# Performance work log

Hardware: AMD Instinct MI355X
Metric: run time of the kernel (lower is better)

The kernel has to match this reference:

```python
import jax, jax.numpy as jnp
import numpy as np

BETA = 0.25

def setup_inputs() -> dict:
    key = jax.random.key(0)
    k1, k2 = jax.random.split(key)
    B, D, H, W = 32, 256, 32, 32
    K = 2048
    latents = jax.random.normal(k1, (B, D, H, W), dtype=jnp.float32)
    # torch init: uniform(-1/K, 1/K)
    embedding_weight = jax.random.uniform(k2, (K, D), dtype=jnp.float32, minval=-1.0 / K, maxval=1.0 / K)
    return {"latents": latents, "embedding_weight": embedding_weight}

def reference(latents, embedding_weight):
    B, D, H, W = latents.shape
    # NCHW -> NHWC -> (N, D)
    x = jnp.transpose(latents, (0, 2, 3, 1)).reshape(-1, D)
    dist = (jnp.sum(x * x, axis=1, keepdims=True)
            - 2.0 * jnp.matmul(x, embedding_weight.T)
            + jnp.sum(embedding_weight * embedding_weight, axis=1))
    embed_ind = jnp.argmin(dist, axis=1)  # argmax of -dist
    quantized = jnp.take(embedding_weight, embed_ind, axis=0)  # (N, D) gather, same math as onehot @ W
    x_nhwc = x.reshape(B, H, W, D)
    q_nhwc = quantized.reshape(B, H, W, D)
    # straight-through-style residual: latents + beta * (sg(quantized) - latents)
    out = x_nhwc + BETA * (jax.lax.stop_gradient(q_nhwc) - x_nhwc)
    out = jnp.transpose(out, (0, 3, 1, 2))  # back to NCHW
    return out, embed_ind.reshape(B, H, W)
```

## Files before the change

kernel.cpp:

```cpp
#include <hip/hip_runtime.h>
#include <math.h>

#define BB 32
#define DD 256
#define KK 2048
#define HW 1024
#define CHW (DD*HW)
#define NN (BB*HW)
#define BETA 0.25f
#define RROWS 32
#define NCAND 8
#define BIAS 0.125f

typedef __attribute__((ext_vector_type(8))) short short8v;
typedef __attribute__((ext_vector_type(4))) float f32x4;

typedef const __attribute__((address_space(1))) void gv_t;
typedef __attribute__((address_space(3))) void lv_t;

__device__ __forceinline__ void gl_lds16(const void* g, void* l) {
    __builtin_amdgcn_global_load_lds((gv_t*)g, (lv_t*)l, 16, 0, 0);
}

__device__ __forceinline__ unsigned bfr(float f) {
    unsigned u = __float_as_uint(f);
    return (u + 0x7FFFu + ((u >> 16) & 1u)) >> 16;
}
__device__ __forceinline__ unsigned bfpack(float lo, float hi) {
    return bfr(lo) | (bfr(hi) << 16);
}

#define BARRIER() do { asm volatile("" ::: "memory"); \
                       __builtin_amdgcn_s_barrier();  \
                       asm volatile("" ::: "memory"); } while (0)

__global__ __launch_bounds__(256) void k_prep(const float* __restrict__ E,
                                              uint4* __restrict__ EbfT,
                                              float* __restrict__ Cref,
                                              float* __restrict__ Ckey) {
    int bid = blockIdx.x;
    if (bid < 256) {
        int u = bid * 256 + threadIdx.x;
        int code = u & 31, kc = (u >> 5) & 3, c = (u >> 7) & 7, t = u >> 10;
        int k = t * 32 + code;
        const float* s = E + ((size_t)k * DD + c * 32 + kc * 8);
        float4 f0 = *reinterpret_cast<const float4*>(s);
        float4 f1 = *reinterpret_cast<const float4*>(s + 4);
        uint4 o;
        o.x = bfpack(f0.x, f0.y); o.y = bfpack(f0.z, f0.w);
        o.z = bfpack(f1.x, f1.y); o.w = bfpack(f1.z, f1.w);
        EbfT[u] = o;
    } else {
        const int w = threadIdx.x >> 6;
        const int lane = threadIdx.x & 63;
        const int k = (bid - 256) * 4 + w;
        float racc = 0.0f;
        if (lane < 16) {
#pragma clang fp contract(off)
            const int j = lane & 7, h = lane >> 3;
            const float* e = E + (size_t)k * DD + h * 128 + j;
            for (int i = 0; i < 16; ++i) {
                float t = e[i * 8];
                racc += t * t;
            }
        }
        float v0 = __shfl(racc, 0, 64),  v1 = __shfl(racc, 1, 64);
        float v2 = __shfl(racc, 2, 64),  v3 = __shfl(racc, 3, 64);
        float v4 = __shfl(racc, 4, 64),  v5 = __shfl(racc, 5, 64);
        float v6 = __shfl(racc, 6, 64),  v7 = __shfl(racc, 7, 64);
        float v8 = __shfl(racc, 8, 64),  v9 = __shfl(racc, 9, 64);
        float va = __shfl(racc, 10, 64), vb = __shfl(racc, 11, 64);
        float vc = __shfl(racc, 12, 64), vd = __shfl(racc, 13, 64);
        float ve = __shfl(racc, 14, 64), vf = __shfl(racc, 15, 64);
        if (lane == 0) {
#pragma clang fp contract(off)
            float lo = ((v0 + v1) + (v2 + v3)) + ((v4 + v5) + (v6 + v7));
            float hi = ((v8 + v9) + (va + vb)) + ((vc + vd) + (ve + vf));
            float res = lo + hi;
            Cref[k] = res;
            Ckey[k] = res + BIAS;
        }
    }
}

__global__ __launch_bounds__(512, 4) void k_screen(
        const float* __restrict__ X, const uint4* __restrict__ EbfT,
        const float* __restrict__ Ckey, uint2* __restrict__ ck)
{
    __shared__ __align__(1024) char lds[36864];

    const int tid = threadIdx.x;
    const int w = tid >> 6;
    const int rg = w >> 1;
    const int cg = w & 1;
    const int lane = tid & 63;
    const int lid = lane & 15, kc = lane >> 4;
    const int bid = blockIdx.x;
    const int half = bid & 1;
    const int tbase = half * 32;
    const int nb = (bid >> 1) * 64;
    const int b = nb >> 10;
    const int hw0 = nb & 1023;

    float* ckl = (float*)(lds + 32768);

    float ckg0 = Ckey[half * 1024 + tid];
    float ckg1 = Ckey[half * 1024 + 512 + tid];

    short8v a[8];
    {
        const float* xb = X + (size_t)b * CHW + (hw0 + rg * 16 + lid);
        #pragma unroll
        for (int c = 0; c < 8; ++c) {
            const float* pp = xb + (size_t)(c * 32 + kc * 8) * HW;
            float f[8];
            #pragma unroll
            for (int j = 0; j < 8; ++j) f[j] = pp[(size_t)j * HW];
            uint4 v;
            v.x = bfpack(f[0], f[1]); v.y = bfpack(f[2], f[3]);
            v.z = bfpack(f[4], f[5]); v.w = bfpack(f[6], f[7]);
            a[c] = *reinterpret_cast<short8v*>(&v);
        }
    }
    ckl[tid] = ckg0;
    ckl[tid + 512] = ckg1;

    auto stage = [&](int t, int p) {
        const uint4* src = EbfT + ((size_t)(tbase + t) * 1024 + w * 128 + lane);
        char* dst = lds + p * 16384 + (w * 128) * 16;
        #pragma unroll
        for (int i = 0; i < 2; ++i)
            gl_lds16(src + i * 64, dst + i * 1024);
    };
    stage(0, 0);
    stage(1, 1);
    asm volatile("s_waitcnt vmcnt(0) lgkmcnt(0)" ::: "memory");
    BARRIER();

    unsigned t1[4], t2[4];
    #pragma unroll
    for (int g = 0; g < 4; ++g) { t1[g] = 0xFFFFFFFFu; t2[g] = 0xFFFFFFFFu; }

    f32x4 acc = (f32x4){0.f, 0.f, 0.f, 0.f};

    int p = 0;
    float pck = 0.f;
    #pragma unroll 1
    for (int tt = 0; tt < 32; ++tt) {
        float ckv = ckl[tt * 32 + cg * 16 + lid];

        if (tt > 0) {
            unsigned tg = (unsigned)(tt - 1);
            #pragma unroll
            for (int g = 0; g < 4; ++g) {
                float s = fmaf(-2.0f, acc[g], pck);
                unsigned key = (__float_as_uint(s) & 0xFFFFFFE0u) | tg;
                unsigned o1 = t1[g];
                unsigned hi = key > o1 ? key : o1;
                t1[g] = key < o1 ? key : o1;
                t2[g] = hi < t2[g] ? hi : t2[g];
                acc[g] = 0.0f;
            }
        }
        pck = ckv;

        const short8v* Ev = reinterpret_cast<const short8v*>(lds + p * 16384);
        #pragma unroll
        for (int c = 0; c < 8; ++c) {
            short8v b0 = Ev[c * 128 + kc * 32 + cg * 16 + lid];
            acc = __builtin_amdgcn_mfma_f32_16x16x32_bf16(a[c], b0, acc, 0, 0, 0);
        }

        BARRIER();
        if (tt < 30) {
            stage(tt + 2, p);
        }
        asm volatile("s_waitcnt vmcnt(0)" ::: "memory");
        BARRIER();
        p ^= 1;
    }
    {
        unsigned tg = 31u;
        #pragma unroll
        for (int g = 0; g < 4; ++g) {
            float s = fmaf(-2.0f, acc[g], pck);
            unsigned key = (__float_as_uint(s) & 0xFFFFFFE0u) | tg;
            unsigned o1 = t1[g];
            unsigned hi = key > o1 ? key : o1;
            t1[g] = key < o1 ? key : o1;
            t2[g] = hi < t2[g] ? hi : t2[g];
        }
    }

    uint2* mb = reinterpret_cast<uint2*>(lds);
    uint2* scr = reinterpret_cast<uint2*>(lds + 16384);
    #pragma unroll
    for (int g = 0; g < 4; ++g) {
        int row = rg * 16 + kc * 4 + g;
        int slot = cg * 16 + lid;
        uint2 v; v.x = t1[g]; v.y = t2[g];
        mb[row * 32 + slot] = v;
    }
    BARRIER();
    if (tid < 256) {
        int row = tid >> 2, q = tid & 3;
        unsigned prev = 0; int prevj = -1;
        for (int i = 0; i < 4; ++i) {
            unsigned cur = 0xFFFFFFFFu; int curj = 0x7FFFFFFF;
            #pragma unroll
            for (int s = 0; s < 8; ++s) {
                int slot = q * 8 + ((s + tid) & 7);
                uint2 kv = mb[row * 32 + slot];
                int j0 = slot * 2;
                { unsigned k2=kv.x; int j=j0;   if ((k2>prev||(k2==prev&&j>prevj)) && (k2<cur||(k2==cur&&j<curj))) {cur=k2;curj=j;} }
                { unsigned k2=kv.y; int j=j0+1; if ((k2>prev||(k2==prev&&j>prevj)) && (k2<cur||(k2==cur&&j<curj))) {cur=k2;curj=j;} }
            }
            uint2 pr; pr.x = cur; pr.y = (unsigned)curj;
            scr[(row * 4 + q) * 4 + i] = pr;
            prev = cur; prevj = curj;
        }
    }
    BARRIER();
    if (tid < 64) {
        unsigned prev = 0; int prevj = -1;
        unsigned short codes[4];
        for (int i = 0; i < 4; ++i) {
            unsigned cur = 0xFFFFFFFFu; int curj = 0x7FFFFFFF;
            for (int m = 0; m < 16; ++m) {
                int mm = (m + tid) & 15;
                uint2 pr = scr[tid * 16 + mm];
                unsigned k2 = pr.x; int j = (int)pr.y;
                if ((k2>prev||(k2==prev&&j>prevj)) && (k2<cur||(k2==cur&&j<curj))) {cur=k2;curj=j;}
            }
            prev = cur; prevj = curj;
            codes[i] = (unsigned short)(half * 1024 + (int)(cur & 31u) * 32 + ((curj >> 1) & 31));
        }
        uint2 o;
        o.x = (unsigned)codes[0] | ((unsigned)codes[1] << 16);
        o.y = (unsigned)codes[2] | ((unsigned)codes[3] << 16);
        ck[(size_t)(nb + tid) * 2 + half] = o;
    }
}

__global__ __launch_bounds__(512) void k_refineout(const float* __restrict__ X,
                                                   const float* __restrict__ E,
                                                   const float* __restrict__ Cref,
                                                   const uint2* __restrict__ ck,
                                                   float* __restrict__ idx_out_f,
                                                   float* __restrict__ out) {
    __shared__ float Xl[RROWS][DD + 4];
    __shared__ float El[RROWS][DD + 4];
    __shared__ int bk_l[RROWS];
    const int tid = threadIdx.x;
    const int n0 = blockIdx.x * RROWS;
    const int b = n0 >> 10;
    const int hw0 = n0 & 1023;
    const float* xbase = X + (size_t)b * CHW + hw0;
    #pragma unroll
    for (int it = 0; it < 16; ++it) {
        int idx = tid + it * 512;
        int d = idx >> 5, rr = idx & 31;
        Xl[rr][d] = xbase[(size_t)d * HW + rr];
    }
    __syncthreads();
    const int r = tid >> 4, c = tid & 15;
    const int sub = c & 7;
    uint4 ck4 = reinterpret_cast<const uint4*>(ck)[n0 + r];
    const unsigned short* cs = reinterpret_cast<const unsigned short*>(&ck4);

    float A;
    {
        float racc;
        {
#pragma clang fp contract(off)
            const int j = c & 7, h = c >> 3;
            const float* xr = &Xl[r][h * 128 + j];
            racc = 0.0f;
            for (int i = 0; i < 16; ++i) {
                float t = xr[i * 8];
                racc += t * t;
            }
        }
        float w1 = __shfl_xor(racc, 1, 16);
        float s1, s2, s4;
        {
#pragma clang fp contract(off)
            s1 = racc + w1;
        }
        float w2 = __shfl_xor(s1, 2, 16);
        {
#pragma clang fp contract(off)
            s2 = s1 + w2;
        }
        float w4 = __shfl_xor(s2, 4, 16);
        {
#pragma clang fp contract(off)
            s4 = s2 + w4;
        }
        float w8 = __shfl_xor(s4, 8, 16);
        {
#pragma clang fp contract(off)
            A = s4 + w8;
        }
    }

    float bd = INFINITY; int bk = 0x7FFFFFFF;
    #pragma unroll
    for (int cc = 0; cc < 4; ++cc) {
        int k = cs[cc * 2 + (c >> 3)] & 2047;
        const float* er = E + (size_t)k * DD;
        double p = 0.0;
        #pragma unroll
        for (int m = 0; m < 8; ++m) {
            float4 ev = *reinterpret_cast<const float4*>(er + m * 32 + sub * 4);
            float4 xv = *reinterpret_cast<const float4*>(&Xl[r][m * 32 + sub * 4]);
            p += (double)xv.x*ev.x + (double)xv.y*ev.y
               + (double)xv.z*ev.z + (double)xv.w*ev.w;
        }
        p += __shfl_xor(p, 1, 64);
        p += __shfl_xor(p, 2, 64);
        p += __shfl_xor(p, 4, 64);
        float dist;
        {
#pragma clang fp contract(off)
            float M  = (float)p;
            float Bt = 2.0f * M;
            float T1 = A - Bt;
            dist = T1 + Cref[k];
        }
        if (dist < bd || (dist == bd && k < bk)) { bd = dist; bk = k; }
    }
    {
        float bd2 = __shfl_xor(bd, 8, 64);
        int   bk2 = __shfl_xor(bk, 8, 64);
        if (bd2 < bd || (bd2 == bd && bk2 < bk)) { bd = bd2; bk = bk2; }
    }
    if (c == 0) {
        bk_l[r] = bk;
        idx_out_f[n0 + r] = (float)bk;
    }
    __syncthreads();
    {
        int kk = bk_l[r];
        const float* er = E + (size_t)kk * DD;
        #pragma unroll
        for (int m = 0; m < 4; ++m)
            *reinterpret_cast<float4*>(&El[r][m * 64 + c * 4]) =
                *reinterpret_cast<const float4*>(er + m * 64 + c * 4);
    }
    __syncthreads();
    {
        const int rr = tid & 31;
        const int d0 = tid >> 5;
        float* ob = out + (size_t)b * CHW + hw0 + rr;
        #pragma unroll
        for (int it = 0; it < 16; ++it) {
            int d = d0 + it * 16;
            float x = Xl[rr][d];
            float qv = El[rr][d];
            ob[(size_t)d * HW] = x + BETA * (qv - x);
        }
    }
}

extern "C" void kernel_launch(void* const* d_in, const int* in_sizes, int n_in,
                              void* d_out, int out_size, void* d_ws, size_t ws_size,
                              hipStream_t stream) {
    const float* lat = (const float*)d_in[0];
    const float* emb = (const float*)d_in[1];
    float* out   = (float*)d_out;
    float* idx_f = out + (size_t)BB * DD * HW;

    char*  ob   = (char*)d_out;
    uint4* EbfT = (uint4*)(ob);

    char* ws = (char*)d_ws;
    float* Ckey = (float*)(ws + 0);
    float* Cref = (float*)(ws + 8192);
    uint2* ck   = (uint2*)(ws + 16384);

    k_prep      <<<768, 256, 0, stream>>>(emb, EbfT, Cref, Ckey);
    k_screen    <<<NN / 64 * 2, 512, 0, stream>>>(lat, EbfT, Ckey, ck);
    k_refineout <<<NN / RROWS, 512, 0, stream>>>(lat, emb, Cref, ck, idx_f, out);
}
```

Baseline: 139.7 us.

## Split refine and output writeback into separate kernels via index buffer

Splits the fused refine+output kernel into two. The refine kernel now only computes the argmin, writing it to a workspace int buffer. A new elementwise kernel reads latents in contiguous float4 chunks, gathers codebook values by index and writes the output. This drops roughly 33KB of LDS and two barriers from the refine kernel, which may raise its occupancy. The cost is one extra launch and a second read of the 32MB latent tensor.

```diff
diff --git a/kernel.cpp b/kernel.cpp
--- a/kernel.cpp
+++ b/kernel.cpp
@@ -242,15 +242,13 @@
     }
 }
 
-__global__ __launch_bounds__(512) void k_refineout(const float* __restrict__ X,
-                                                   const float* __restrict__ E,
-                                                   const float* __restrict__ Cref,
-                                                   const uint2* __restrict__ ck,
-                                                   float* __restrict__ idx_out_f,
-                                                   float* __restrict__ out) {
+__global__ __launch_bounds__(512) void k_refine(const float* __restrict__ X,
+                                                const float* __restrict__ E,
+                                                const float* __restrict__ Cref,
+                                                const uint2* __restrict__ ck,
+                                                float* __restrict__ idx_out_f,
+                                                int* __restrict__ ind) {
     __shared__ float Xl[RROWS][DD + 4];
-    __shared__ float El[RROWS][DD + 4];
-    __shared__ int bk_l[RROWS];
     const int tid = threadIdx.x;
     const int n0 = blockIdx.x * RROWS;
     const int b = n0 >> 10;
@@ -336,31 +334,34 @@
         if (bd2 < bd || (bd2 == bd && bk2 < bk)) { bd = bd2; bk = bk2; }
     }
     if (c == 0) {
-        bk_l[r] = bk;
+        ind[n0 + r] = bk;
         idx_out_f[n0 + r] = (float)bk;
     }
-    __syncthreads();
-    {
-        int kk = bk_l[r];
-        const float* er = E + (size_t)kk * DD;
-        #pragma unroll
-        for (int m = 0; m < 4; ++m)
-            *reinterpret_cast<float4*>(&El[r][m * 64 + c * 4]) =
-                *reinterpret_cast<const float4*>(er + m * 64 + c * 4);
-    }
-    __syncthreads();
-    {
-        const int rr = tid & 31;
-        const int d0 = tid >> 5;
-        float* ob = out + (size_t)b * CHW + hw0 + rr;
-        #pragma unroll
-        for (int it = 0; it < 16; ++it) {
-            int d = d0 + it * 16;
-            float x = Xl[rr][d];
-            float qv = El[rr][d];
-            ob[(size_t)d * HW] = x + BETA * (qv - x);
-        }
-    }
+}
+
+__global__ __launch_bounds__(256) void k_out(const float* __restrict__ X,
+                                             const float* __restrict__ E,
+                                             const int* __restrict__ ind,
+                                             float* __restrict__ out) {
+    int gid = blockIdx.x * 256 + threadIdx.x;
+    int e0 = gid << 2;
+    int hw = e0 & 1023;
+    int d  = (e0 >> 10) & 255;
+    int b  = e0 >> 18;
+    int n0 = (b << 10) | hw;
+
+    float4 x = *reinterpret_cast<const float4*>(X + e0);
+    int4  iv = *reinterpret_cast<const int4*>(ind + n0);
+    float q0 = E[(size_t)iv.x * DD + d];
+    float q1 = E[(size_t)iv.y * DD + d];
+    float q2 = E[(size_t)iv.z * DD + d];
+    float q3 = E[(size_t)iv.w * DD + d];
+    float4 r;
+    r.x = x.x + BETA * (q0 - x.x);
+    r.y = x.y + BETA * (q1 - x.y);
+    r.z = x.z + BETA * (q2 - x.z);
+    r.w = x.w + BETA * (q3 - x.w);
+    *reinterpret_cast<float4*>(out + e0) = r;
 }
 
 extern "C" void kernel_launch(void* const* d_in, const int* in_sizes, int n_in,
@@ -378,8 +379,10 @@
     float* Ckey = (float*)(ws + 0);
     float* Cref = (float*)(ws + 8192);
     uint2* ck   = (uint2*)(ws + 16384);
-
-    k_prep      <<<768, 256, 0, stream>>>(emb, EbfT, Cref, Ckey);
-    k_screen    <<<NN / 64 * 2, 512, 0, stream>>>(lat, EbfT, Ckey, ck);
-    k_refineout <<<NN / RROWS, 512, 0, stream>>>(lat, emb, Cref, ck, idx_f, out);
-}
+    int*   ind  = (int*)(ws + 540672);
+
+    k_prep   <<<768, 256, 0, stream>>>(emb, EbfT, Cref, Ckey);
+    k_screen <<<NN / 64 * 2, 512, 0, stream>>>(lat, EbfT, Ckey, ck);
+    k_refine <<<NN / RROWS, 512, 0, stream>>>(lat, emb, Cref, ck, idx_f, ind);
+    k_out    <<<(BB * DD * HW) / 4 / 256, 256, 0, stream>>>(lat, emb, ind, out);
+}
```

Result: faster. 134.3 us (-3.8%).
